# Performance work log

Measured on AMD Instinct MI355X. Metric: run time of the kernel, lower is better.

The kernel has to match this reference:

```python
import jax, jax.numpy as jnp
import numpy as np

EPS = 1e-6

def _log_g(x):
    # log of continuous g(x) = where(x>=0, x+0.5, sigmoid(x)) from minGRU paper
    return jnp.where(x >= 0, jnp.log(jax.nn.relu(x) + 0.5), -jax.nn.softplus(-x))

def setup_inputs() -> dict:
    key = jax.random.key(0)
    ks = jax.random.split(key, 4)
    B, S, D, E = 4, 2048, 1024, 8
    scale = D ** -0.5
    return {
        "inputs": jax.random.normal(ks[0], (B, S, D), dtype=jnp.float32),
        "norm_weight": jnp.ones((D,), jnp.float32),
        "router_w": jax.random.normal(ks[1], (E, D), jnp.float32) * scale,
        "router_b": jnp.zeros((E,), jnp.float32),
        "w_hg": jax.random.normal(ks[2], (E, 2 * D, D), jnp.float32) * scale,
        "w_out": jax.random.normal(ks[3], (E, D, D), jnp.float32) * scale,
    }

def reference(inputs, norm_weight, router_w, router_b, w_hg, w_out):
    D = inputs.shape[-1]
    # --- RMSNorm ---
    x = inputs * jax.lax.rsqrt(jnp.mean(inputs * inputs, axis=-1, keepdims=True) + EPS) * norm_weight
    # --- SMEAR: per-sample soft merge of expert weights via mean-pooled routing ---
    probs = jax.nn.softmax(jnp.mean(x, axis=1) @ router_w.T + router_b, axis=-1)  # [B,E]
    W_hg = jnp.einsum('be,ekd->bkd', probs, w_hg)    # [B,2D,D] merged to_hidden_and_gate
    W_out = jnp.einsum('be,eod->bod', probs, w_out)  # [B,D,D]  merged to_out
    # --- minGRU with merged weights (log-space parallel scan, no initial state) ---
    hg = jnp.einsum('bsd,bkd->bsk', x, W_hg)         # [B,S,2D]
    hidden, gate = hg[..., :D], hg[..., D:]
    log_coeffs = -jax.nn.softplus(gate)                      # log(1 - z_t)
    log_values = -jax.nn.softplus(-gate) + _log_g(hidden)    # log z_t + log g(h~_t)
    a_star = jnp.cumsum(log_coeffs, axis=1)
    log_h = a_star + jax.lax.cumlogsumexp(log_values - a_star, axis=1)
    h = jnp.exp(log_h)                               # [B,S,D] recurrent states
    new_state = h[:, -1:]                            # [B,1,D]
    out = jnp.einsum('bsk,bok->bso', h, W_out)       # proj_out
    aux_loss = jnp.zeros((), inputs.dtype)
    return (out + inputs, new_state, aux_loss)
```

## Files before the change

kernel.cpp:

```cpp
#include <hip/hip_runtime.h>
#include <hip/hip_bf16.h>
#include <hip/hip_fp16.h>

#define B_  4
#define S_  2048
#define D_  1024
#define E_  8
#define K2_ 2048

#define CHUNKS 64
#define CLEN   32

typedef __attribute__((ext_vector_type(8))) short short8;
typedef __attribute__((ext_vector_type(4))) float floatx4;

__device__ __forceinline__ void gld16(const void* g, const void* l) {
    __builtin_amdgcn_global_load_lds(
        (const __attribute__((address_space(1))) unsigned int*)g,
        (__attribute__((address_space(3))) unsigned int*)l, 16, 0, 0);
}

__device__ __forceinline__ unsigned short f2bf(float f) {
    unsigned int u = __float_as_uint(f);
    u += 0x7fffu + ((u >> 16) & 1u);
    return (unsigned short)(u >> 16);
}

__global__ void rmsnorm_k(const float* __restrict__ in, const float* __restrict__ nw,
                          __hip_bfloat16* __restrict__ x) {
    int b = blockIdx.y, s = blockIdx.x, t = threadIdx.x;
    const float4* row = (const float4*)(in + ((size_t)b * S_ + s) * D_);
    float4 v = row[t];
    float ss = v.x * v.x + v.y * v.y + v.z * v.z + v.w * v.w;
#pragma unroll
    for (int o = 32; o > 0; o >>= 1) ss += __shfl_down(ss, o, 64);
    __shared__ float ls[4];
    if ((t & 63) == 0) ls[t >> 6] = ss;
    __syncthreads();
    float tot = ls[0] + ls[1] + ls[2] + ls[3];
    float rs = rsqrtf(tot * (1.0f / (float)D_) + 1e-6f);
    float4 w = ((const float4*)nw)[t];
    ushort4 o;
    o.x = f2bf(v.x * rs * w.x); o.y = f2bf(v.y * rs * w.y);
    o.z = f2bf(v.z * rs * w.z); o.w = f2bf(v.w * rs * w.w);
    ((ushort4*)(x + ((size_t)b * S_ + s) * D_))[t] = o;
}

__global__ void xsum_k(const __hip_bfloat16* __restrict__ x, float* __restrict__ xs) {
    int d = blockIdx.x * 256 + threadIdx.x;
    int b = blockIdx.y;
    int s0 = blockIdx.z * 128;
    const __hip_bfloat16* p = x + ((size_t)b * S_ + s0) * D_ + d;
    float acc = 0.0f;
#pragma unroll 4
    for (int s = 0; s < 128; s++) { acc += __bfloat162float(*p); p += D_; }
    atomicAdd(&xs[b * D_ + d], acc);
}

__global__ void router_k(const float* __restrict__ xs, const float* __restrict__ rw,
                         const float* __restrict__ rb, float* __restrict__ probs,
                         float* __restrict__ aux) {
    int t = threadIdx.x;
    if (t == 255) *aux = 0.0f;
    int pair = t >> 3, sub = t & 7;
    int b = pair >> 3, e = pair & 7;
    float acc = 0.0f;
#pragma unroll 8
    for (int d = sub; d < D_; d += 8) acc += xs[b * D_ + d] * rw[e * D_ + d];
#pragma unroll
    for (int o = 4; o > 0; o >>= 1) acc += __shfl_down(acc, o, 8);
    __shared__ float lg[32];
    if (sub == 0) lg[pair] = acc * (1.0f / (float)S_) + rb[e];
    __syncthreads();
    if (t < 4) {
        float m = -1e30f;
        for (int e2 = 0; e2 < 8; e2++) m = fmaxf(m, lg[t * 8 + e2]);
        float ssum = 0.0f; float ex[8];
        for (int e2 = 0; e2 < 8; e2++) { ex[e2] = expf(lg[t * 8 + e2] - m); ssum += ex[e2]; }
        for (int e2 = 0; e2 < 8; e2++) probs[t * 8 + e2] = ex[e2] / ssum;
    }
}

__global__ void mix_k(const float* __restrict__ probs, const float* __restrict__ whg_e,
                      const float* __restrict__ wout_e, __hip_bfloat16* __restrict__ Whg,
                      __hip_bfloat16* __restrict__ Wout) {
    __shared__ float P[32];
    int t = threadIdx.x;
    if (t < 32) P[t] = probs[t];
    __syncthreads();
    size_t i4 = (size_t)blockIdx.x * 256 + t;
    const size_t T1q = (size_t)K2_ * D_ / 4;
    const size_t T2q = (size_t)D_ * D_ / 4;
    float4 a0 = {0,0,0,0}, a1 = {0,0,0,0}, a2 = {0,0,0,0}, a3 = {0,0,0,0};
    if (i4 < T1q) {
        const float4* src = (const float4*)whg_e;
#pragma unroll
        for (int e = 0; e < 8; e++) {
            float4 wv = src[(size_t)e * T1q + i4];
            float p0 = P[e], p1 = P[8 + e], p2 = P[16 + e], p3 = P[24 + e];
            a0.x += p0 * wv.x; a0.y += p0 * wv.y; a0.z += p0 * wv.z; a0.w += p0 * wv.w;
            a1.x += p1 * wv.x; a1.y += p1 * wv.y; a1.z += p1 * wv.z; a1.w += p1 * wv.w;
            a2.x += p2 * wv.x; a2.y += p2 * wv.y; a2.z += p2 * wv.z; a2.w += p2 * wv.w;
            a3.x += p3 * wv.x; a3.y += p3 * wv.y; a3.z += p3 * wv.z; a3.w += p3 * wv.w;
        }
        ushort4* dst = (ushort4*)Whg;
        ushort4 o;
        o.x = f2bf(a0.x); o.y = f2bf(a0.y); o.z = f2bf(a0.z); o.w = f2bf(a0.w);
        dst[0 * T1q + i4] = o;
        o.x = f2bf(a1.x); o.y = f2bf(a1.y); o.z = f2bf(a1.z); o.w = f2bf(a1.w);
        dst[1 * T1q + i4] = o;
        o.x = f2bf(a2.x); o.y = f2bf(a2.y); o.z = f2bf(a2.z); o.w = f2bf(a2.w);
        dst[2 * T1q + i4] = o;
        o.x = f2bf(a3.x); o.y = f2bf(a3.y); o.z = f2bf(a3.z); o.w = f2bf(a3.w);
        dst[3 * T1q + i4] = o;
    } else {
        size_t j4 = i4 - T1q;
        const float4* src = (const float4*)wout_e;
#pragma unroll
        for (int e = 0; e < 8; e++) {
            float4 wv = src[(size_t)e * T2q + j4];
            float p0 = P[e], p1 = P[8 + e], p2 = P[16 + e], p3 = P[24 + e];
            a0.x += p0 * wv.x; a0.y += p0 * wv.y; a0.z += p0 * wv.z; a0.w += p0 * wv.w;
            a1.x += p1 * wv.x; a1.y += p1 * wv.y; a1.z += p1 * wv.z; a1.w += p1 * wv.w;
            a2.x += p2 * wv.x; a2.y += p2 * wv.y; a2.z += p2 * wv.z; a2.w += p2 * wv.w;
            a3.x += p3 * wv.x; a3.y += p3 * wv.y; a3.z += p3 * wv.z; a3.w += p3 * wv.w;
        }
        ushort4* dst = (ushort4*)Wout;
        ushort4 o;
        o.x = f2bf(a0.x); o.y = f2bf(a0.y); o.z = f2bf(a0.z); o.w = f2bf(a0.w);
        dst[0 * T2q + j4] = o;
        o.x = f2bf(a1.x); o.y = f2bf(a1.y); o.z = f2bf(a1.z); o.w = f2bf(a1.w);
        dst[1 * T2q + j4] = o;
        o.x = f2bf(a2.x); o.y = f2bf(a2.y); o.z = f2bf(a2.z); o.w = f2bf(a2.w);
        dst[2 * T2q + j4] = o;
        o.x = f2bf(a3.x); o.y = f2bf(a3.y); o.z = f2bf(a3.z); o.w = f2bf(a3.w);
        dst[3 * T2q + j4] = o;
    }
}

__global__ __launch_bounds__(512, 2) void gemm_hg_cv(
    const __hip_bfloat16* __restrict__ A, const __hip_bfloat16* __restrict__ Bm,
    __half2* __restrict__ cv) {
    const int K = D_;
    int bz = blockIdx.z;
    A  += (size_t)bz * S_ * D_;
    Bm += (size_t)bz * K2_ * D_;
    __half2* CV = cv + (size_t)bz * S_ * D_;
    int id = blockIdx.x;
    int sw = (id & 7) * 8 + (id >> 3);
    int m0 = (sw >> 3) * 256, n0 = (sw & 7) * 128;
    __shared__ __hip_bfloat16 lA[2][2][256][32];
    __shared__ __hip_bfloat16 lBh[2][2][128][32];
    __shared__ __hip_bfloat16 lBg[2][2][128][32];
    int t = threadIdx.x;
    int w = t >> 6, lane = t & 63;
    int lm = lane & 15, quad = lane >> 4;
    int wr = w >> 1, wc = w & 1;
    floatx4 acch[4][4] = {};
    floatx4 accg[4][4] = {};
    int rloc = lane >> 2;
    int swz4 = ((lane & 3) ^ ((lane >> 3) & 3)) * 16;
    int pch  = (quad ^ ((lm >> 1) & 3)) * 16;

    const __hip_bfloat16* Bh = Bm;
    const __hip_bfloat16* Bg = Bm + (size_t)D_ * K;

    const char* pA0 = (const char*)(A  + (size_t)(m0 + (w * 2 + 0) * 16 + rloc) * K) + swz4;
    const char* pA1 = (const char*)(A  + (size_t)(m0 + (w * 2 + 1) * 16 + rloc) * K) + swz4;
    const char* pBhp = (const char*)(Bh + (size_t)(n0 + w * 16 + rloc) * K) + swz4;
    const char* pBgp = (const char*)(Bg + (size_t)(n0 + w * 16 + rloc) * K) + swz4;

    auto stage_kh0 = [&](int bb) {
        gld16(pA0, &lA[bb][0][(w * 2 + 0) * 16][0]);
        gld16(pA1, &lA[bb][0][(w * 2 + 1) * 16][0]);
        gld16(pBhp, &lBh[bb][0][w * 16][0]);
        gld16(pBgp, &lBg[bb][0][w * 16][0]);
    };
    auto stage_kh1 = [&](int bb) {
        gld16(pA0 + 64, &lA[bb][1][(w * 2 + 0) * 16][0]);
        gld16(pA1 + 64, &lA[bb][1][(w * 2 + 1) * 16][0]);
        gld16(pBhp + 64, &lBh[bb][1][w * 16][0]);
        gld16(pBgp + 64, &lBg[bb][1][w * 16][0]);
        pA0 += 128; pA1 += 128; pBhp += 128; pBgp += 128;
    };

    stage_kh0(0); stage_kh1(0);
    for (int kt = 0; kt < 16; kt++) {
        int cur = kt & 1, nxt = cur ^ 1;
        bool pre = (kt < 15);
        asm volatile("s_waitcnt vmcnt(4)" ::: "memory");
        __builtin_amdgcn_s_barrier();
        asm volatile("" ::: "memory");
        {
            short8 af[4], bh[4], bg[4];
#pragma unroll
            for (int i = 0; i < 4; i++)
                af[i] = *(const short8*)((const char*)&lA[cur][0][wr * 64 + i * 16 + lm][0] + pch);
#pragma unroll
            for (int j = 0; j < 4; j++) {
                bh[j] = *(const short8*)((const char*)&lBh[cur][0][wc * 64 + j * 16 + lm][0] + pch);
                bg[j] = *(const short8*)((const char*)&lBg[cur][0][wc * 64 + j * 16 + lm][0] + pch);
            }
            if (pre) stage_kh0(nxt);
            __builtin_amdgcn_s_setprio(1);
#pragma unroll
            for (int i = 0; i < 4; i++)
#pragma unroll
                for (int j = 0; j < 4; j++) {
                    acch[i][j] = __builtin_amdgcn_mfma_f32_16x16x32_bf16(af[i], bh[j], acch[i][j], 0, 0, 0);
                    accg[i][j] = __builtin_amdgcn_mfma_f32_16x16x32_bf16(af[i], bg[j], accg[i][j], 0, 0, 0);
                }
            __builtin_amdgcn_s_setprio(0);
        }
        if (pre) asm volatile("s_waitcnt vmcnt(4)" ::: "memory");
        else     asm volatile("s_waitcnt vmcnt(0)" ::: "memory");
        __builtin_amdgcn_s_barrier();
        asm volatile("" ::: "memory");
        {
            short8 af[4], bh[4], bg[4];
#pragma unroll
            for (int i = 0; i < 4; i++)
                af[i] = *(const short8*)((const char*)&lA[cur][1][wr * 64 + i * 16 + lm][0] + pch);
#pragma unroll
            for (int j = 0; j < 4; j++) {
                bh[j] = *(const short8*)((const char*)&lBh[cur][1][wc * 64 + j * 16 + lm][0] + pch);
                bg[j] = *(const short8*)((const char*)&lBg[cur][1][wc * 64 + j * 16 + lm][0] + pch);
            }
            if (pre) stage_kh1(nxt);
            __builtin_amdgcn_s_setprio(1);
#pragma unroll
            for (int i = 0; i < 4; i++)
#pragma unroll
                for (int j = 0; j < 4; j++) {
                    acch[i][j] = __builtin_amdgcn_mfma_f32_16x16x32_bf16(af[i], bh[j], acch[i][j], 0, 0, 0);
                    accg[i][j] = __builtin_amdgcn_mfma_f32_16x16x32_bf16(af[i], bg[j], accg[i][j], 0, 0, 0);
                }
            __builtin_amdgcn_s_setprio(0);
        }
    }
#pragma unroll
    for (int i = 0; i < 4; i++) {
#pragma unroll
        for (int j = 0; j < 4; j++) {
#pragma unroll
            for (int r = 0; r < 4; r++) {
                int m = m0 + wr * 64 + i * 16 + quad * 4 + r;
                int n = n0 + wc * 64 + j * 16 + lm;
                float hid = acch[i][j][r];
                float g   = accg[i][j][r];
                float eg  = expf(g);
                float c   = 1.0f / (1.0f + eg);
                float sg  = 1.0f - c;
                float gfn = (hid >= 0.0f) ? (hid + 0.5f)
                                          : (1.0f / (1.0f + expf(-hid)));
                CV[(size_t)m * D_ + n] = __floats2half2_rn(c, sg * gfn);
            }
        }
    }
}

__global__ __launch_bounds__(512, 2) void gemm_bf16_bt(
    const __hip_bfloat16* __restrict__ A, const __hip_bfloat16* __restrict__ Bm,
    float* __restrict__ C, const float* __restrict__ R,
    int M, int N, int K, size_t sa, size_t sb, size_t sc, size_t sr) {
    int bz = blockIdx.z;
    A += (size_t)bz * sa; Bm += (size_t)bz * sb; C += (size_t)bz * sc;
    if (R) R += (size_t)bz * sr;
    int id = blockIdx.x;
    int sw = (id & 7) * 8 + (id >> 3);
    int m0 = (sw >> 3) * 256, n0 = (sw & 7) * 128;
    __shared__ __hip_bfloat16 lA[2][2][256][32];
    __shared__ __hip_bfloat16 lB[2][2][128][32];
    int t = threadIdx.x;
    int w = t >> 6, lane = t & 63;
    int lm = lane & 15, quad = lane >> 4;
    int wr = w >> 1, wc = w & 1;
    floatx4 acc[4][4] = {};
    int rloc = lane >> 2;
    int swz4 = ((lane & 3) ^ ((lane >> 3) & 3)) * 16;
    int pch  = (quad ^ ((lm >> 1) & 3)) * 16;

    const char* pA0 = (const char*)(A  + (size_t)(m0 + (w * 2 + 0) * 16 + rloc) * K) + swz4;
    const char* pA1 = (const char*)(A  + (size_t)(m0 + (w * 2 + 1) * 16 + rloc) * K) + swz4;
    const char* pB0 = (const char*)(Bm + (size_t)(n0 + w * 16 + rloc) * K) + swz4;

    auto stage_kh0 = [&](int bb) {
        gld16(pA0, &lA[bb][0][(w * 2 + 0) * 16][0]);
        gld16(pA1, &lA[bb][0][(w * 2 + 1) * 16][0]);
        gld16(pB0, &lB[bb][0][w * 16][0]);
    };
    auto stage_kh1 = [&](int bb) {
        gld16(pA0 + 64, &lA[bb][1][(w * 2 + 0) * 16][0]);
        gld16(pA1 + 64, &lA[bb][1][(w * 2 + 1) * 16][0]);
        gld16(pB0 + 64, &lB[bb][1][w * 16][0]);
        pA0 += 128; pA1 += 128; pB0 += 128;
    };

    stage_kh0(0); stage_kh1(0);
    int NT = K / 64;
    for (int kt = 0; kt < NT; kt++) {
        int cur = kt & 1, nxt = cur ^ 1;
        bool pre = (kt < NT - 1);
        asm volatile("s_waitcnt vmcnt(3)" ::: "memory");
        __builtin_amdgcn_s_barrier();
        asm volatile("" ::: "memory");
        {
            short8 af[4], bf[4];
#pragma unroll
            for (int i = 0; i < 4; i++)
                af[i] = *(const short8*)((const char*)&lA[cur][0][wr * 64 + i * 16 + lm][0] + pch);
#pragma unroll
            for (int j = 0; j < 4; j++)
                bf[j] = *(const short8*)((const char*)&lB[cur][0][wc * 64 + j * 16 + lm][0] + pch);
            if (pre) stage_kh0(nxt);
            __builtin_amdgcn_s_setprio(1);
#pragma unroll
            for (int i = 0; i < 4; i++)
#pragma unroll
                for (int j = 0; j < 4; j++)
                    acc[i][j] = __builtin_amdgcn_mfma_f32_16x16x32_bf16(af[i], bf[j], acc[i][j], 0, 0, 0);
            __builtin_amdgcn_s_setprio(0);
        }
        if (pre) asm volatile("s_waitcnt vmcnt(3)" ::: "memory");
        else     asm volatile("s_waitcnt vmcnt(0)" ::: "memory");
        __builtin_amdgcn_s_barrier();
        asm volatile("" ::: "memory");
        {
            short8 af[4], bf[4];
#pragma unroll
            for (int i = 0; i < 4; i++)
                af[i] = *(const short8*)((const char*)&lA[cur][1][wr * 64 + i * 16 + lm][0] + pch);
#pragma unroll
            for (int j = 0; j < 4; j++)
                bf[j] = *(const short8*)((const char*)&lB[cur][1][wc * 64 + j * 16 + lm][0] + pch);
            if (pre) stage_kh1(nxt);
            __builtin_amdgcn_s_setprio(1);
#pragma unroll
            for (int i = 0; i < 4; i++)
#pragma unroll
                for (int j = 0; j < 4; j++)
                    acc[i][j] = __builtin_amdgcn_mfma_f32_16x16x32_bf16(af[i], bf[j], acc[i][j], 0, 0, 0);
            __builtin_amdgcn_s_setprio(0);
        }
    }
#pragma unroll
    for (int i = 0; i < 4; i++) {
#pragma unroll
        for (int j = 0; j < 4; j++) {
#pragma unroll
            for (int r = 0; r < 4; r++) {
                int m = m0 + wr * 64 + i * 16 + quad * 4 + r;
                int n = n0 + wc * 64 + j * 16 + lm;
                float v = acc[i][j][r];
                if (R) v += R[(size_t)m * N + n];
                __builtin_nontemporal_store(v, &C[(size_t)m * N + n]);
            }
        }
    }
}

__global__ void scanA_k(const __half2* __restrict__ cv, float* __restrict__ Cc,
                        float* __restrict__ Vc) {
    int c = blockIdx.x, b = blockIdx.y, t = threadIdx.x;
    const float4* p = (const float4*)(cv + (size_t)(b * S_ + c * CLEN) * D_) + t;
    float P0 = 1, P1 = 1, P2 = 1, P3 = 1;
    float V0 = 0, V1 = 0, V2 = 0, V3 = 0;
#pragma unroll 4
    for (int s = 0; s < CLEN; s++) {
        float4 raw = p[(size_t)s * (D_ / 4)];
        const __half2* e = (const __half2*)&raw;
        float c0 = __low2float(e[0]), v0 = __high2float(e[0]);
        float c1 = __low2float(e[1]), v1 = __high2float(e[1]);
        float c2 = __low2float(e[2]), v2 = __high2float(e[2]);
        float c3 = __low2float(e[3]), v3 = __high2float(e[3]);
        P0 *= c0; V0 = fmaf(c0, V0, v0);
        P1 *= c1; V1 = fmaf(c1, V1, v1);
        P2 *= c2; V2 = fmaf(c2, V2, v2);
        P3 *= c3; V3 = fmaf(c3, V3, v3);
    }
    size_t q = ((size_t)(b * CHUNKS + c)) * (D_ / 4) + t;
    ((float4*)Cc)[q] = make_float4(P0, P1, P2, P3);
    ((float4*)Vc)[q] = make_float4(V0, V1, V2, V3);
}

__global__ void scanC_k(const __half2* __restrict__ cv, const float* __restrict__ Cc,
                        const float* __restrict__ Vc,
                        __hip_bfloat16* __restrict__ hout, float* __restrict__ ns) {
    int c = blockIdx.x, b = blockIdx.y, t = threadIdx.x;
    float h0 = 0, h1 = 0, h2 = 0, h3 = 0;
#pragma unroll 4
    for (int cc = 0; cc < c; cc++) {
        size_t q = ((size_t)(b * CHUNKS + cc)) * (D_ / 4) + t;
        float4 C4 = ((const float4*)Cc)[q];
        float4 V4 = ((const float4*)Vc)[q];
        h0 = fmaf(C4.x, h0, V4.x); h1 = fmaf(C4.y, h1, V4.y);
        h2 = fmaf(C4.z, h2, V4.z); h3 = fmaf(C4.w, h3, V4.w);
    }
    const float4* p = (const float4*)(cv + (size_t)(b * S_ + c * CLEN) * D_) + t;
    ushort4* hq = (ushort4*)(hout + (size_t)(b * S_ + c * CLEN) * D_) + t;
#pragma unroll 4
    for (int s = 0; s < CLEN; s++) {
        float4 raw = p[(size_t)s * (D_ / 4)];
        const __half2* e = (const __half2*)&raw;
        h0 = fmaf(__low2float(e[0]), h0, __high2float(e[0]));
        h1 = fmaf(__low2float(e[1]), h1, __high2float(e[1]));
        h2 = fmaf(__low2float(e[2]), h2, __high2float(e[2]));
        h3 = fmaf(__low2float(e[3]), h3, __high2float(e[3]));
        ushort4 o;
        o.x = f2bf(h0); o.y = f2bf(h1); o.z = f2bf(h2); o.w = f2bf(h3);
        hq[(size_t)s * (D_ / 4)] = o;
    }
    if (c == CHUNKS - 1)
        ((float4*)(ns + (size_t)b * D_))[t] = make_float4(h0, h1, h2, h3);
}

extern "C" void kernel_launch(void* const* d_in, const int* in_sizes, int n_in,
                              void* d_out_v, int out_size, void* d_ws, size_t ws_size,
                              hipStream_t stream) {
    const float* inputs = (const float*)d_in[0];
    const float* nw     = (const float*)d_in[1];
    const float* rw     = (const float*)d_in[2];
    const float* rb     = (const float*)d_in[3];
    const float* whg_e  = (const float*)d_in[4];
    const float* wout_e = (const float*)d_in[5];
    float* out = (float*)d_out_v;

    float* ws = (float*)d_ws;
    __half2*        cv      = (__half2*)ws;
    __hip_bfloat16* x_bf    = (__hip_bfloat16*)(ws + 8388608);
    __hip_bfloat16* h_bf    = (__hip_bfloat16*)(ws + 12582912);
    __hip_bfloat16* Whg_bf  = (__hip_bfloat16*)(ws + 16777216);
    __hip_bfloat16* Wout_bf = (__hip_bfloat16*)(ws + 20971520);
    float* xsum  = ws + 23068672;
    float* probs = ws + 23072768;
    float* Cc    = ws + 23072800;
    float* Vc    = ws + 23334944;

    hipMemsetAsync(xsum, 0, (size_t)B_ * D_ * sizeof(float), stream);

    rmsnorm_k<<<dim3(S_, B_), 256, 0, stream>>>(inputs, nw, x_bf);
    xsum_k<<<dim3(D_ / 256, B_, 16), 256, 0, stream>>>(x_bf, xsum);
    router_k<<<1, 256, 0, stream>>>(xsum, rw, rb, probs,
                                    out + (size_t)B_ * S_ * D_ + (size_t)B_ * D_);
    mix_k<<<3072, 256, 0, stream>>>(probs, whg_e, wout_e, Whg_bf, Wout_bf);

    gemm_hg_cv<<<dim3(64, 1, B_), 512, 0, stream>>>(x_bf, Whg_bf, cv);

    scanA_k<<<dim3(CHUNKS, B_), 256, 0, stream>>>(cv, Cc, Vc);
    scanC_k<<<dim3(CHUNKS, B_), 256, 0, stream>>>(
        cv, Cc, Vc, h_bf, out + (size_t)B_ * S_ * D_);

    gemm_bf16_bt<<<dim3(64, 1, B_), 512, 0, stream>>>(
        h_bf, Wout_bf, out, inputs, S_, D_, D_,
        (size_t)S_ * D_, (size_t)D_ * D_, (size_t)S_ * D_, (size_t)S_ * D_);
}
```

Measured before the change: 295.3 us.

## Fuse mean-pool into RMSNorm and fold router softmax into weight-mixing kernel

The RMSNorm kernel now handles 16 rows per block and accumulates the per-feature sum in registers, then adds it to the mean-pool buffer with atomics. This removes the separate xsum kernel that re-read the bf16 activations. The router logits and softmax are recomputed redundantly in every block of the weight-mixing kernel, which removes the single-block router launch. The trade is redundant router work across 3072 blocks, which re-read the 32 KB router weights and the pooled sums, plus two extra syncthreads per row in the norm kernel. The pooled mean is now summed from fp32 values rather than bf16-rounded ones, which also shifts the routing numerics slightly.

```diff
diff --git a/kernel.cpp b/kernel.cpp
--- a/kernel.cpp
+++ b/kernel.cpp
@@ -26,68 +26,63 @@
     return (unsigned short)(u >> 16);
 }
 
-__global__ void rmsnorm_k(const float* __restrict__ in, const float* __restrict__ nw,
-                          __hip_bfloat16* __restrict__ x) {
-    int b = blockIdx.y, s = blockIdx.x, t = threadIdx.x;
-    const float4* row = (const float4*)(in + ((size_t)b * S_ + s) * D_);
-    float4 v = row[t];
-    float ss = v.x * v.x + v.y * v.y + v.z * v.z + v.w * v.w;
-#pragma unroll
-    for (int o = 32; o > 0; o >>= 1) ss += __shfl_down(ss, o, 64);
+__global__ void rmsnorm16_k(const float* __restrict__ in, const float* __restrict__ nw,
+                            __hip_bfloat16* __restrict__ x, float* __restrict__ xs) {
+    int b = blockIdx.y, s0 = blockIdx.x * 16, t = threadIdx.x;
+    float4 w = ((const float4*)nw)[t];
+    float a0 = 0, a1 = 0, a2 = 0, a3 = 0;
     __shared__ float ls[4];
-    if ((t & 63) == 0) ls[t >> 6] = ss;
-    __syncthreads();
-    float tot = ls[0] + ls[1] + ls[2] + ls[3];
-    float rs = rsqrtf(tot * (1.0f / (float)D_) + 1e-6f);
-    float4 w = ((const float4*)nw)[t];
-    ushort4 o;
-    o.x = f2bf(v.x * rs * w.x); o.y = f2bf(v.y * rs * w.y);
-    o.z = f2bf(v.z * rs * w.z); o.w = f2bf(v.w * rs * w.w);
-    ((ushort4*)(x + ((size_t)b * S_ + s) * D_))[t] = o;
-}
-
-__global__ void xsum_k(const __hip_bfloat16* __restrict__ x, float* __restrict__ xs) {
-    int d = blockIdx.x * 256 + threadIdx.x;
-    int b = blockIdx.y;
-    int s0 = blockIdx.z * 128;
-    const __hip_bfloat16* p = x + ((size_t)b * S_ + s0) * D_ + d;
-    float acc = 0.0f;
-#pragma unroll 4
-    for (int s = 0; s < 128; s++) { acc += __bfloat162float(*p); p += D_; }
-    atomicAdd(&xs[b * D_ + d], acc);
-}
-
-__global__ void router_k(const float* __restrict__ xs, const float* __restrict__ rw,
-                         const float* __restrict__ rb, float* __restrict__ probs,
-                         float* __restrict__ aux) {
+    for (int r = 0; r < 16; r++) {
+        int s = s0 + r;
+        float4 v = ((const float4*)(in + ((size_t)b * S_ + s) * D_))[t];
+        float ss = v.x * v.x + v.y * v.y + v.z * v.z + v.w * v.w;
+#pragma unroll
+        for (int o = 32; o > 0; o >>= 1) ss += __shfl_down(ss, o, 64);
+        if ((t & 63) == 0) ls[t >> 6] = ss;
+        __syncthreads();
+        float tot = ls[0] + ls[1] + ls[2] + ls[3];
+        __syncthreads();
+        float rs = rsqrtf(tot * (1.0f / (float)D_) + 1e-6f);
+        float x0 = v.x * rs * w.x, x1 = v.y * rs * w.y;
+        float x2 = v.z * rs * w.z, x3 = v.w * rs * w.w;
+        a0 += x0; a1 += x1; a2 += x2; a3 += x3;
+        ushort4 o;
+        o.x = f2bf(x0); o.y = f2bf(x1); o.z = f2bf(x2); o.w = f2bf(x3);
+        ((ushort4*)(x + ((size_t)b * S_ + s) * D_))[t] = o;
+    }
+    float* base = xs + (size_t)b * D_ + t * 4;
+    atomicAdd(base + 0, a0); atomicAdd(base + 1, a1);
+    atomicAdd(base + 2, a2); atomicAdd(base + 3, a3);
+}
+
+__global__ void mix_k(const float* __restrict__ xs, const float* __restrict__ rw,
+                      const float* __restrict__ rb,
+                      const float* __restrict__ whg_e, const float* __restrict__ wout_e,
+                      __hip_bfloat16* __restrict__ Whg, __hip_bfloat16* __restrict__ Wout,
+                      float* __restrict__ aux) {
+    __shared__ float P[32];
+    __shared__ float lg[32];
     int t = threadIdx.x;
-    if (t == 255) *aux = 0.0f;
-    int pair = t >> 3, sub = t & 7;
-    int b = pair >> 3, e = pair & 7;
-    float acc = 0.0f;
+    {
+        int pair = t >> 3, sub = t & 7;
+        int b = pair >> 3, e = pair & 7;
+        float acc = 0.0f;
 #pragma unroll 8
-    for (int d = sub; d < D_; d += 8) acc += xs[b * D_ + d] * rw[e * D_ + d];
-#pragma unroll
-    for (int o = 4; o > 0; o >>= 1) acc += __shfl_down(acc, o, 8);
-    __shared__ float lg[32];
-    if (sub == 0) lg[pair] = acc * (1.0f / (float)S_) + rb[e];
-    __syncthreads();
-    if (t < 4) {
-        float m = -1e30f;
-        for (int e2 = 0; e2 < 8; e2++) m = fmaxf(m, lg[t * 8 + e2]);
-        float ssum = 0.0f; float ex[8];
-        for (int e2 = 0; e2 < 8; e2++) { ex[e2] = expf(lg[t * 8 + e2] - m); ssum += ex[e2]; }
-        for (int e2 = 0; e2 < 8; e2++) probs[t * 8 + e2] = ex[e2] / ssum;
-    }
-}
-
-__global__ void mix_k(const float* __restrict__ probs, const float* __restrict__ whg_e,
-                      const float* __restrict__ wout_e, __hip_bfloat16* __restrict__ Whg,
-                      __hip_bfloat16* __restrict__ Wout) {
-    __shared__ float P[32];
-    int t = threadIdx.x;
-    if (t < 32) P[t] = probs[t];
-    __syncthreads();
+        for (int d = sub; d < D_; d += 8) acc += xs[b * D_ + d] * rw[e * D_ + d];
+#pragma unroll
+        for (int o = 4; o > 0; o >>= 1) acc += __shfl_down(acc, o, 8);
+        if (sub == 0) lg[pair] = acc * (1.0f / (float)S_) + rb[e];
+        __syncthreads();
+        if (t < 4) {
+            float m = -1e30f;
+            for (int e2 = 0; e2 < 8; e2++) m = fmaxf(m, lg[t * 8 + e2]);
+            float ssum = 0.0f; float ex[8];
+            for (int e2 = 0; e2 < 8; e2++) { ex[e2] = expf(lg[t * 8 + e2] - m); ssum += ex[e2]; }
+            for (int e2 = 0; e2 < 8; e2++) P[t * 8 + e2] = ex[e2] / ssum;
+        }
+        if (blockIdx.x == 0 && t == 255) *aux = 0.0f;
+        __syncthreads();
+    }
     size_t i4 = (size_t)blockIdx.x * 256 + t;
     const size_t T1q = (size_t)K2_ * D_ / 4;
     const size_t T2q = (size_t)D_ * D_ / 4;
@@ -432,17 +427,15 @@
     __hip_bfloat16* Whg_bf  = (__hip_bfloat16*)(ws + 16777216);
     __hip_bfloat16* Wout_bf = (__hip_bfloat16*)(ws + 20971520);
     float* xsum  = ws + 23068672;
-    float* probs = ws + 23072768;
     float* Cc    = ws + 23072800;
     float* Vc    = ws + 23334944;
 
     hipMemsetAsync(xsum, 0, (size_t)B_ * D_ * sizeof(float), stream);
 
-    rmsnorm_k<<<dim3(S_, B_), 256, 0, stream>>>(inputs, nw, x_bf);
-    xsum_k<<<dim3(D_ / 256, B_, 16), 256, 0, stream>>>(x_bf, xsum);
-    router_k<<<1, 256, 0, stream>>>(xsum, rw, rb, probs,
+    rmsnorm16_k<<<dim3(S_ / 16, B_), 256, 0, stream>>>(inputs, nw, x_bf, xsum);
+
+    mix_k<<<3072, 256, 0, stream>>>(xsum, rw, rb, whg_e, wout_e, Whg_bf, Wout_bf,
                                     out + (size_t)B_ * S_ * D_ + (size_t)B_ * D_);
-    mix_k<<<3072, 256, 0, stream>>>(probs, whg_e, wout_e, Whg_bf, Wout_bf);
 
     gemm_hg_cv<<<dim3(64, 1, B_), 512, 0, stream>>>(x_bf, Whg_bf, cv);
 
```

Measured after the change: 322.9 us. 9.4% more time.
